# Kernel optimization log

Hardware: AMD Instinct MI355X
Metric: run time of the kernel (lower is better)

The kernel has to match this reference:

```python
import jax, jax.numpy as jnp
import numpy as np


def setup_inputs() -> dict:
    key = jax.random.key(0)
    ks = jax.random.split(key, 6)
    B, L, V, D, H, C = 2048, 200, 50000, 300, 32, 3
    x = jax.random.randint(ks[0], (B, L), 0, V)
    lengths = jax.random.randint(ks[1], (B,), 1, L + 1)
    emb_table = jax.random.normal(ks[2], (V, D), dtype=jnp.float32)
    W1 = jax.random.normal(ks[3], (D, H), dtype=jnp.float32) * (1.0 / np.sqrt(D))
    b1 = jnp.zeros((H,), dtype=jnp.float32)
    W2 = jax.random.normal(ks[4], (H, C), dtype=jnp.float32) * (1.0 / np.sqrt(H))
    b2 = jnp.zeros((C,), dtype=jnp.float32)
    return {"x": x, "lengths": lengths, "emb_table": emb_table,
            "W1": W1, "b1": b1, "W2": W2, "b2": b2}


def reference(x, lengths, emb_table, W1, b1, W2, b2):
    # Embedding gather: [B, L, D]
    emb = emb_table[x]
    # Length-normalized sum over the (padded) sequence, matching the torch
    # loop which sums ALL L positions and divides by lengths[i].
    rep = emb.sum(axis=1) / lengths[:, None].astype(emb.dtype)  # [B, D]
    h = jax.nn.relu(rep @ W1 + b1)  # [B, 32]
    logits = h @ W2 + b2            # [B, C]
    return logits
```

## Files before the change

kernel.cpp:

```cpp
#include <hip/hip_runtime.h>
#include <hip/hip_bf16.h>

typedef __attribute__((ext_vector_type(8))) short short8;
typedef __attribute__((ext_vector_type(4))) short short4v;
typedef __attribute__((ext_vector_type(4))) float floatx4;

__device__ float Pbuf[50000 * 32];

__device__ __forceinline__ short tobf16(float f) {
    unsigned u = __builtin_bit_cast(unsigned, f);
    u += 0x7fffu + ((u >> 16) & 1u);
    return (short)(u >> 16);
}

#define APAD 336

__global__ __launch_bounds__(256, 2) void project_kernel(
        const float* __restrict__ E, const float* __restrict__ W1, int V) {
    __shared__ __align__(16) short w1t[32][APAD];
    __shared__ __align__(16) short atile[2][32][APAD];

    int tid   = threadIdx.x;
    int b     = blockIdx.x;
    int tiles = (V + 31) >> 5;
    int NT    = (tiles - b + 511) >> 9;

    for (int idx = tid; idx < 2 * 32 * 20; idx += 256) {
        int bufi = idx / (32 * 20);
        int rem  = idx % (32 * 20);
        atile[bufi][rem / 20][300 + rem % 20] = 0;
    }
    for (int idx = tid; idx < 32 * 20; idx += 256)
        w1t[idx / 20][300 + idx % 20] = 0;

    int arow = tid >> 3;
    int aq   = tid & 7;

    floatx4 wreg[10];
#pragma unroll
    for (int r = 0; r < 10; ++r) {
        int ch = tid + (r << 8);
        if (ch < 2400) wreg[r] = *(const floatx4*)(W1 + (size_t)ch * 4);
    }
    floatx4 areg[10];
    {
        int nrows0 = min(32, V - (b << 5));
        const float* eb = E + ((size_t)b << 5) * 300;
#pragma unroll
        for (int j = 0; j < 10; ++j) {
            int c = aq + 8 * j;
            if (c < 75 && arow < nrows0)
                areg[j] = *(const floatx4*)(eb + (size_t)arow * 300 + c * 4);
        }
    }
#pragma unroll
    for (int r = 0; r < 10; ++r) {
        int ch = tid + (r << 8);
        if (ch < 2400) {
            int flat = ch * 4;
            int k = flat >> 5, n0 = flat & 31;
#pragma unroll
            for (int jj = 0; jj < 4; ++jj) w1t[n0 + jj][k] = tobf16(wreg[r][jj]);
        }
    }
    {
        int nrows0 = min(32, V - (b << 5));
#pragma unroll
        for (int j = 0; j < 10; ++j) {
            int c = aq + 8 * j;
            if (c < 75 && arow < nrows0) {
                short4v s;
#pragma unroll
                for (int jj = 0; jj < 4; ++jj) s[jj] = tobf16(areg[j][jj]);
                *(short4v*)&atile[0][arow][c * 4] = s;
            }
        }
    }
    __syncthreads();

    int lane   = tid & 63;
    int w      = tid >> 6;
    int m      = lane & 15;
    int quad   = lane >> 4;
    int rowsub = (w & 1) << 4;
    int ncol0  = (w >> 1) << 4;

    short8 bfrag[10];
#pragma unroll
    for (int s = 0; s < 10; ++s)
        bfrag[s] = *(const short8*)&w1t[ncol0 + m][s * 32 + quad * 8];

    for (int i = 0; i < NT; ++i) {
        int t   = b + (i << 9);
        int cur = i & 1;
        bool pf = (i + 1 < NT);
        int tn  = t + 512;
        int nrowsN = pf ? min(32, V - (tn << 5)) : 0;

        const float* eb2 = E + ((size_t)tn << 5) * 300;
#pragma unroll
        for (int j = 0; j < 10; ++j) {
            int c = aq + 8 * j;
            if (pf && c < 75 && arow < nrowsN)
                areg[j] = *(const floatx4*)(eb2 + (size_t)arow * 300 + c * 4);
        }
        __builtin_amdgcn_sched_barrier(0);

        int nrows = min(32, V - (t << 5));
        floatx4 acc = {0.f, 0.f, 0.f, 0.f};
        if (rowsub < nrows) {
#pragma unroll
            for (int s = 0; s < 10; ++s) {
                short8 a = *(const short8*)&atile[cur][rowsub + m][s * 32 + quad * 8];
                acc = __builtin_amdgcn_mfma_f32_16x16x32_bf16(a, bfrag[s], acc, 0, 0, 0);
            }
        }

        if (pf) {
#pragma unroll
            for (int j = 0; j < 10; ++j) {
                int c = aq + 8 * j;
                if (c < 75 && arow < nrowsN) {
                    short4v s;
#pragma unroll
                    for (int jj = 0; jj < 4; ++jj) s[jj] = tobf16(areg[j][jj]);
                    *(short4v*)&atile[cur ^ 1][arow][c * 4] = s;
                }
            }
        }

        if (rowsub < nrows) {
#pragma unroll
            for (int r = 0; r < 4; ++r) {
                int row = (t << 5) + rowsub + quad * 4 + r;
                Pbuf[(size_t)row * 32 + ncol0 + m] = acc[r];
            }
        }

        __syncthreads();
    }
}

__global__ __launch_bounds__(256) void pool_mlp_kernel(
        const int* __restrict__ x, const int* __restrict__ lengths,
        const float* __restrict__ b1, const float* __restrict__ W2,
        const float* __restrict__ b2, float* __restrict__ out, int L, int C) {
    __shared__ int   xs[512];
    __shared__ float red[4][32];
    int b    = blockIdx.x;
    int w    = threadIdx.x >> 6;
    int lane = threadIdx.x & 63;
    int h    = lane & 31;
    int th   = lane >> 5;

    const int* xrow = x + (size_t)b * L;
    for (int i = threadIdx.x; i < L; i += 256) xs[i] = xrow[i];
    __syncthreads();

    int Lw    = (L + 3) >> 2;
    int start = w * Lw;
    int end   = min(start + Lw, L);

    float acc = 0.f;
    int t = start;
    for (; t + 8 <= end; t += 8) {
        int i0 = xs[t + th];
        int i1 = xs[t + 2 + th];
        int i2 = xs[t + 4 + th];
        int i3 = xs[t + 6 + th];
        float v0 = Pbuf[(size_t)i0 * 32 + h];
        float v1 = Pbuf[(size_t)i1 * 32 + h];
        float v2 = Pbuf[(size_t)i2 * 32 + h];
        float v3 = Pbuf[(size_t)i3 * 32 + h];
        acc += v0; acc += v1; acc += v2; acc += v3;
    }
    for (; t < end; t += 2) {
        int tt = t + th;
        if (tt < end) acc += Pbuf[(size_t)xs[tt] * 32 + h];
    }
    acc += __shfl_xor(acc, 32, 64);
    if (lane < 32) red[w][h] = acc;
    __syncthreads();

    if (threadIdx.x < 32) {
        float s    = red[0][h] + red[1][h] + red[2][h] + red[3][h];
        float lenf = (float)lengths[b];
        float hv   = fmaxf(s / lenf + b1[h], 0.f);
        for (int c = 0; c < C; ++c) {
            float p = hv * W2[h * C + c];
            p += __shfl_xor(p, 16, 64);
            p += __shfl_xor(p, 8, 64);
            p += __shfl_xor(p, 4, 64);
            p += __shfl_xor(p, 2, 64);
            p += __shfl_xor(p, 1, 64);
            if (threadIdx.x == 0) out[(size_t)b * C + c] = p + b2[c];
        }
    }
}

__global__ void naive_dnn(const int* __restrict__ x, const int* __restrict__ len,
                          const float* __restrict__ emb, const float* __restrict__ W1,
                          const float* __restrict__ b1, const float* __restrict__ W2,
                          const float* __restrict__ b2, float* __restrict__ out,
                          int L, int V, int D, int H, int C) {
    __shared__ float srep[2048];
    __shared__ float sh[256];
    int b = blockIdx.x;
    float lenf = (float)len[b];
    for (int d = threadIdx.x; d < D; d += blockDim.x) {
        float acc = 0.f;
        for (int l = 0; l < L; ++l) {
            int idx = x[(size_t)b * L + l];
            acc += emb[(size_t)idx * D + d];
        }
        srep[d] = acc / lenf;
    }
    __syncthreads();
    for (int hh = threadIdx.x; hh < H; hh += blockDim.x) {
        float a = b1[hh];
        for (int d = 0; d < D; ++d) a += srep[d] * W1[(size_t)d * H + hh];
        sh[hh] = fmaxf(a, 0.f);
    }
    __syncthreads();
    for (int c = threadIdx.x; c < C; c += blockDim.x) {
        float a = b2[c];
        for (int hh = 0; hh < H; ++hh) a += sh[hh] * W2[hh * C + c];
        out[(size_t)b * C + c] = a;
    }
}

extern "C" void kernel_launch(void* const* d_in, const int* in_sizes, int n_in,
                              void* d_out, int out_size, void* d_ws, size_t ws_size,
                              hipStream_t stream) {
    const int*   x       = (const int*)d_in[0];
    const int*   lengths = (const int*)d_in[1];
    const float* emb     = (const float*)d_in[2];
    const float* W1      = (const float*)d_in[3];
    const float* b1      = (const float*)d_in[4];
    const float* W2      = (const float*)d_in[5];
    const float* b2      = (const float*)d_in[6];
    float* out = (float*)d_out;

    int B = in_sizes[1];
    int L = in_sizes[0] / B;
    int H = in_sizes[4];
    int C = in_sizes[6];
    int D = in_sizes[3] / H;
    int V = in_sizes[2] / D;

    bool fast = (D == 300) && (H == 32) && (V == 50000) && (L <= 512);
    if (fast) {
        int tiles  = (V + 31) >> 5;
        int blocks = min(512, tiles);
        project_kernel<<<blocks, 256, 0, stream>>>(emb, W1, V);
        pool_mlp_kernel<<<B, 256, 0, stream>>>(x, lengths, b1, W2, b2, out, L, C);
    } else {
        naive_dnn<<<B, 256, 0, stream>>>(x, lengths, emb, W1, b1, W2, b2, out,
                                         L, V, D, H, C);
    }
}
```

Baseline: 112.7 us.

## Deepen embedding prefetch to two tiles ahead and widen pool gather unroll

The projection kernel now keeps two register staging sets and issues global loads for the tile two iterations ahead, alternating buffers through a lambda body. This gives the loads more time in flight before they are converted to bf16 and stored to LDS. The pooling kernel also gains a 16-wide unrolled gather loop so more independent Pbuf loads are outstanding per warp. The cost is higher register pressure, with 80 extra VGPRs for staging, which may reduce occupancy under launch_bounds(256,2).

New measurement: 113.9 us. About the same (+1.0%).

```diff
diff --git a/kernel.cpp b/kernel.cpp
--- a/kernel.cpp
+++ b/kernel.cpp
@@ -36,21 +36,33 @@
     int arow = tid >> 3;
     int aq   = tid & 7;
 
+    floatx4 rsA[10], rsB[10];
+
     floatx4 wreg[10];
 #pragma unroll
     for (int r = 0; r < 10; ++r) {
         int ch = tid + (r << 8);
         if (ch < 2400) wreg[r] = *(const floatx4*)(W1 + (size_t)ch * 4);
     }
-    floatx4 areg[10];
     {
-        int nrows0 = min(32, V - (b << 5));
+        int nr = min(32, V - (b << 5));
         const float* eb = E + ((size_t)b << 5) * 300;
 #pragma unroll
         for (int j = 0; j < 10; ++j) {
             int c = aq + 8 * j;
-            if (c < 75 && arow < nrows0)
-                areg[j] = *(const floatx4*)(eb + (size_t)arow * 300 + c * 4);
+            if (c < 75 && arow < nr)
+                rsA[j] = *(const floatx4*)(eb + (size_t)arow * 300 + c * 4);
+        }
+    }
+    {
+        int t1 = b + 512;
+        int nr = min(32, V - (t1 << 5));
+        const float* eb = E + ((size_t)t1 << 5) * 300;
+#pragma unroll
+        for (int j = 0; j < 10; ++j) {
+            int c = aq + 8 * j;
+            if (c < 75 && arow < nr)
+                rsB[j] = *(const floatx4*)(eb + (size_t)arow * 300 + c * 4);
         }
     }
 #pragma unroll
@@ -64,14 +76,14 @@
         }
     }
     {
-        int nrows0 = min(32, V - (b << 5));
+        int nr = min(32, V - (b << 5));
 #pragma unroll
         for (int j = 0; j < 10; ++j) {
             int c = aq + 8 * j;
-            if (c < 75 && arow < nrows0) {
+            if (c < 75 && arow < nr) {
                 short4v s;
 #pragma unroll
-                for (int jj = 0; jj < 4; ++jj) s[jj] = tobf16(areg[j][jj]);
+                for (int jj = 0; jj < 4; ++jj) s[jj] = tobf16(rsA[j][jj]);
                 *(short4v*)&atile[0][arow][c * 4] = s;
             }
         }
@@ -90,19 +102,20 @@
     for (int s = 0; s < 10; ++s)
         bfrag[s] = *(const short8*)&w1t[ncol0 + m][s * 32 + quad * 8];
 
-    for (int i = 0; i < NT; ++i) {
+    auto body = [&](int i, floatx4 (&rs_issue)[10], floatx4 (&rs_cons)[10]) {
         int t   = b + (i << 9);
         int cur = i & 1;
-        bool pf = (i + 1 < NT);
-        int tn  = t + 512;
-        int nrowsN = pf ? min(32, V - (tn << 5)) : 0;
-
-        const float* eb2 = E + ((size_t)tn << 5) * 300;
-#pragma unroll
-        for (int j = 0; j < 10; ++j) {
-            int c = aq + 8 * j;
-            if (pf && c < 75 && arow < nrowsN)
-                areg[j] = *(const floatx4*)(eb2 + (size_t)arow * 300 + c * 4);
+
+        int t2 = t + 1024;
+        if (t2 < tiles) {
+            int nr2 = min(32, V - (t2 << 5));
+            const float* eb2 = E + ((size_t)t2 << 5) * 300;
+#pragma unroll
+            for (int j = 0; j < 10; ++j) {
+                int c = aq + 8 * j;
+                if (c < 75 && arow < nr2)
+                    rs_issue[j] = *(const floatx4*)(eb2 + (size_t)arow * 300 + c * 4);
+            }
         }
         __builtin_amdgcn_sched_barrier(0);
 
@@ -116,14 +129,16 @@
             }
         }
 
-        if (pf) {
+        int t1 = t + 512;
+        if (t1 < tiles) {
+            int nr1 = min(32, V - (t1 << 5));
 #pragma unroll
             for (int j = 0; j < 10; ++j) {
                 int c = aq + 8 * j;
-                if (c < 75 && arow < nrowsN) {
+                if (c < 75 && arow < nr1) {
                     short4v s;
 #pragma unroll
-                    for (int jj = 0; jj < 4; ++jj) s[jj] = tobf16(areg[j][jj]);
+                    for (int jj = 0; jj < 4; ++jj) s[jj] = tobf16(rs_cons[j][jj]);
                     *(short4v*)&atile[cur ^ 1][arow][c * 4] = s;
                 }
             }
@@ -136,8 +151,12 @@
                 Pbuf[(size_t)row * 32 + ncol0 + m] = acc[r];
             }
         }
-
         __syncthreads();
+    };
+
+    for (int i = 0; i < NT; i += 2) {
+        body(i, rsA, rsB);
+        if (i + 1 < NT) body(i + 1, rsB, rsA);
     }
 }
 
@@ -163,6 +182,16 @@
 
     float acc = 0.f;
     int t = start;
+    for (; t + 16 <= end; t += 16) {
+        int   idx[8];
+        float v[8];
+#pragma unroll
+        for (int k = 0; k < 8; ++k) idx[k] = xs[t + 2 * k + th];
+#pragma unroll
+        for (int k = 0; k < 8; ++k) v[k] = Pbuf[(size_t)idx[k] * 32 + h];
+#pragma unroll
+        for (int k = 0; k < 8; ++k) acc += v[k];
+    }
     for (; t + 8 <= end; t += 8) {
         int i0 = xs[t + th];
         int i1 = xs[t + 2 + th];
@@ -250,9 +279,7 @@
 
     bool fast = (D == 300) && (H == 32) && (V == 50000) && (L <= 512);
     if (fast) {
-        int tiles  = (V + 31) >> 5;
-        int blocks = min(512, tiles);
-        project_kernel<<<blocks, 256, 0, stream>>>(emb, W1, V);
+        project_kernel<<<512, 256, 0, stream>>>(emb, W1, V);
         pool_mlp_kernel<<<B, 256, 0, stream>>>(x, lengths, b1, W2, b2, out, L, C);
     } else {
         naive_dnn<<<B, 256, 0, stream>>>(x, lengths, emb, W1, b1, W2, b2, out,
```
